# Optimization experiments

Hardware: AMD Instinct MI355X
Metric: run time of the kernel (lower is better)

Reference implementation:

```python
import jax, jax.numpy as jnp
import numpy as np

DIM = 1024
HEADS = 16
DIM_HEAD = 64
INNER = HEADS * DIM_HEAD  # 1024
SCALE = DIM_HEAD ** -0.5


def setup_inputs() -> dict:
    key = jax.random.key(0)
    k_x, k_qkv, k_ow, k_ob = jax.random.split(key, 4)
    B, N = 4, 2048
    x = jax.random.normal(k_x, (B, N, DIM), dtype=jnp.float32)
    # nn.Linear weights stored as [out, in] in torch; keep [in, out] for x @ W.
    w_qkv = jax.random.normal(k_qkv, (DIM, 3 * INNER), dtype=jnp.float32) * (DIM ** -0.5)
    w_out = jax.random.normal(k_ow, (INNER, DIM), dtype=jnp.float32) * (INNER ** -0.5)
    b_out = jax.random.normal(k_ob, (DIM,), dtype=jnp.float32) * 0.01
    return {"x": x, "w_qkv": w_qkv, "w_out": w_out, "b_out": b_out}


def reference(x, w_qkv, w_out, b_out):
    B, N, _ = x.shape
    qkv = x @ w_qkv  # [B, N, 3*inner]
    q, k, v = jnp.split(qkv, 3, axis=-1)
    # [B, N, inner] -> [B, H, N, dh]
    def to_heads(t):
        return t.reshape(B, N, HEADS, DIM_HEAD).transpose(0, 2, 1, 3)
    q, k, v = to_heads(q), to_heads(k), to_heads(v)
    attn = jnp.einsum("bhqd,bhkd->bhqk", q, k) * SCALE  # [B, H, N, N]
    attn = jax.nn.softmax(attn, axis=-1)
    out = jnp.einsum("bhqk,bhkd->bhqd", attn, v)  # [B, H, N, dh]
    out = out.transpose(0, 2, 1, 3).reshape(B, N, INNER)
    return out @ w_out + b_out
```

## Files before the change

### kernel.cpp

```cpp
#include <hip/hip_runtime.h>
#include <hip/hip_bf16.h>
#include <stdint.h>

typedef __attribute__((ext_vector_type(4))) float f32x4;
typedef __attribute__((ext_vector_type(16))) float f32x16;
typedef __attribute__((ext_vector_type(8))) short s16x8;
typedef __attribute__((ext_vector_type(4))) short s16x4;
typedef __attribute__((ext_vector_type(4))) unsigned int u32x4;

#define DEV static __device__ __forceinline__

constexpr int B_ = 4, H_ = 16, N_ = 2048;
constexpr float CL_ = 0.18033688011112042f;

DEV short f2bf(float x) {
  __hip_bfloat16 h = __float2bfloat16(x);
  return *reinterpret_cast<short*>(&h);
}

DEV uint32_t cvtpk(float lo, float hi) {
  uint32_t r;
  asm("v_cvt_pk_bf16_f32 %0, %1, %2" : "=v"(r) : "v"(lo), "v"(hi));
  return r;
}

DEV void gload16(const void* g, void* l) {
  __builtin_amdgcn_global_load_lds((const __attribute__((address_space(1))) void*)g,
                                   (__attribute__((address_space(3))) void*)l, 16, 0, 0);
}

__global__ void k_prep(const float* __restrict__ x, short* __restrict__ xb,
                       const float* __restrict__ wqkv, short* __restrict__ wqkvT,
                       const float* __restrict__ wout, short* __restrict__ woutT) {
  __shared__ short t[64][72];
  int bid = blockIdx.x, tid = threadIdx.x;
  if (bid < 4096) {
    int i = (bid * 256 + tid) * 8;
    const float4* p = reinterpret_cast<const float4*>(x + i);
    float4 a = p[0], b = p[1];
    s16x8 o;
    o[0] = f2bf(a.x); o[1] = f2bf(a.y); o[2] = f2bf(a.z); o[3] = f2bf(a.w);
    o[4] = f2bf(b.x); o[5] = f2bf(b.y); o[6] = f2bf(b.z); o[7] = f2bf(b.w);
    *reinterpret_cast<s16x8*>(xb + i) = o;
    return;
  }
  const float* W;
  short* WT;
  int R = 1024, C, r0, c0;
  if (bid < 4864) {
    int id = bid - 4096;
    W = wqkv; WT = wqkvT; C = 3072;
    c0 = (id % 48) * 64; r0 = (id / 48) * 64;
  } else {
    int id = bid - 4864;
    W = wout; WT = woutT; C = 1024;
    c0 = (id % 16) * 64; r0 = (id / 16) * 64;
  }
  int r = tid >> 2, cp = (tid & 3) * 16;
  const float4* s4 = reinterpret_cast<const float4*>(W + (size_t)(r0 + r) * C + c0 + cp);
  float4 f0 = s4[0], f1 = s4[1], f2 = s4[2], f3 = s4[3];
  short* tr = &t[r][cp];
  tr[0] = f2bf(f0.x); tr[1] = f2bf(f0.y); tr[2]  = f2bf(f0.z); tr[3]  = f2bf(f0.w);
  tr[4] = f2bf(f1.x); tr[5] = f2bf(f1.y); tr[6]  = f2bf(f1.z); tr[7]  = f2bf(f1.w);
  tr[8] = f2bf(f2.x); tr[9] = f2bf(f2.y); tr[10] = f2bf(f2.z); tr[11] = f2bf(f2.w);
  tr[12] = f2bf(f3.x); tr[13] = f2bf(f3.y); tr[14] = f2bf(f3.z); tr[15] = f2bf(f3.w);
  __syncthreads();
  int cc = tid >> 2, rp = (tid & 3) * 16;
  short buf[16];
#pragma unroll
  for (int i = 0; i < 16; ++i) buf[i] = t[rp + i][cc];
  short* dst = WT + (size_t)(c0 + cc) * R + r0 + rp;
  *reinterpret_cast<s16x8*>(dst) = *reinterpret_cast<s16x8*>(buf);
  *reinterpret_cast<s16x8*>(dst + 8) = *reinterpret_cast<s16x8*>(buf + 8);
}

__global__ __launch_bounds__(512, 2)
void k_gemm0(const short* __restrict__ A, const short* __restrict__ BT,
             short* __restrict__ oq, short* __restrict__ ok, short* __restrict__ ovT) {
  __shared__ __align__(16) char smem[98304];
  constexpr int NT = 32;
  const int tid = threadIdx.x;
  const int m0 = blockIdx.x * 128, n0 = blockIdx.y * 256;
  const int lane = tid & 63, w = tid >> 6, g = (lane >> 4) & 3, c = lane & 15;
  const int wm = w & 1, wn = w >> 1;
  f32x4 acc[4][4] = {};
  const int ra = tid >> 2, ca = (tid & 3) * 8;
  const int rb1 = ra + 128;
  const short* gA = A + (size_t)(m0 + ra) * 1024 + ca;
  const short* gB0 = BT + (size_t)(n0 + ra) * 1024 + ca;
  const short* gB1 = BT + (size_t)(n0 + rb1) * 1024 + ca;
#define STAGE0(T)                                                   \
  {                                                                 \
    char* nb = smem + ((T) & 3) * 24576;                            \
    gload16(gA + (T) * 32, nb + tid * 16);                          \
    gload16(gB0 + (T) * 32, nb + 8192 + tid * 16);                  \
    gload16(gB1 + (T) * 32, nb + 8192 + (tid + 512) * 16);          \
  }
  STAGE0(0);
  STAGE0(1);
  for (int t = 0; t < NT; ++t) {
    if (t + 1 < NT) {
      asm volatile("s_waitcnt vmcnt(3)" ::: "memory");
    } else {
      asm volatile("s_waitcnt vmcnt(0)" ::: "memory");
    }
    __builtin_amdgcn_s_barrier();
    __builtin_amdgcn_sched_barrier(0);
    if (t + 2 < NT) STAGE0(t + 2);
    const char* sb = smem + (t & 3) * 24576;
    s16x8 af[4], bf[4];
#pragma unroll
    for (int i = 0; i < 4; ++i)
      af[i] = *reinterpret_cast<const s16x8*>(sb + (wm * 64 + i * 16 + c) * 64 + g * 16);
#pragma unroll
    for (int j = 0; j < 4; ++j)
      bf[j] = *reinterpret_cast<const s16x8*>(sb + 8192 + (wn * 64 + j * 16 + c) * 64 + g * 16);
    __builtin_amdgcn_s_setprio(1);
#pragma unroll
    for (int i = 0; i < 4; ++i)
#pragma unroll
      for (int j = 0; j < 4; ++j)
        acc[i][j] = __builtin_amdgcn_mfma_f32_16x16x32_bf16(af[i], bf[j], acc[i][j], 0, 0, 0);
    __builtin_amdgcn_s_setprio(0);
  }
#undef STAGE0
#pragma unroll
  for (int j = 0; j < 4; ++j) {
    int ncol = n0 + wn * 64 + j * 16 + c;
    int part = ncol >> 10;
    int c10 = ncol & 1023;
    int h = c10 >> 6, d = c10 & 63;
    if (part == 2) {
#pragma unroll
      for (int i = 0; i < 4; ++i) {
        int mrow = m0 + wm * 64 + i * 16 + g * 4;
        int b = mrow >> 11, nr = mrow & 2047;
        uint2 pk;
        pk.x = cvtpk(acc[i][j][0], acc[i][j][1]);
        pk.y = cvtpk(acc[i][j][2], acc[i][j][3]);
        *reinterpret_cast<uint2*>(ovT + ((size_t)((b * H_ + h) * 64 + d) * N_ + nr)) = pk;
      }
    } else {
      short* dst0 = (part == 0) ? oq : ok;
      float qs = (part == 0) ? CL_ : 1.0f;
#pragma unroll
      for (int i = 0; i < 4; ++i) {
#pragma unroll
        for (int r = 0; r < 4; ++r) {
          int mrow = m0 + wm * 64 + i * 16 + g * 4 + r;
          int b = mrow >> 11, nr = mrow & 2047;
          dst0[((size_t)((b * H_ + h) * N_ + nr) << 6) + d] = f2bf(acc[i][j][r] * qs);
        }
      }
    }
  }
}

__global__ __launch_bounds__(256, 2)
void k_gemm1(const short* __restrict__ A, const short* __restrict__ BT,
             int M, int N, int K, const float* __restrict__ bias, float* __restrict__ out) {
  __shared__ short As[128 * 32];
  __shared__ short Bs[128 * 32];
  const int tid = threadIdx.x;
  const int m0 = blockIdx.x * 128, n0 = blockIdx.y * 128;
  const int lane = tid & 63, w = tid >> 6, g = lane >> 4, c = lane & 15;
  const int wr = w >> 1, wc = w & 1;
  f32x4 acc[4][4] = {};
  const int trow = tid >> 2, tk = (tid & 3) * 8;
  const short* ga = A + (size_t)(m0 + trow) * K + tk;
  const short* gb = BT + (size_t)(n0 + trow) * K + tk;
  short* la = As + tid * 8;
  short* lb = Bs + tid * 8;
  for (int k0 = 0; k0 < K; k0 += 32) {
    gload16(ga + k0, la);
    gload16(ga + (size_t)64 * K + k0, la + 2048);
    gload16(gb + k0, lb);
    gload16(gb + (size_t)64 * K + k0, lb + 2048);
    __syncthreads();
    s16x8 af[4], bf[4];
#pragma unroll
    for (int i = 0; i < 4; ++i)
      af[i] = *reinterpret_cast<const s16x8*>(As + (wr * 64 + i * 16 + c) * 32 + g * 8);
#pragma unroll
    for (int j = 0; j < 4; ++j)
      bf[j] = *reinterpret_cast<const s16x8*>(Bs + (wc * 64 + j * 16 + c) * 32 + g * 8);
#pragma unroll
    for (int i = 0; i < 4; ++i)
#pragma unroll
      for (int j = 0; j < 4; ++j)
        acc[i][j] = __builtin_amdgcn_mfma_f32_16x16x32_bf16(af[i], bf[j], acc[i][j], 0, 0, 0);
    __syncthreads();
  }
#pragma unroll
  for (int bj = 0; bj < 4; ++bj) {
    int ncol = n0 + wc * 64 + bj * 16 + c;
    float bb = bias[ncol];
#pragma unroll
    for (int ai = 0; ai < 4; ++ai) {
#pragma unroll
      for (int r = 0; r < 4; ++r) {
        int mrow = m0 + wr * 64 + ai * 16 + g * 4 + r;
        out[(size_t)mrow * N + ncol] = acc[ai][bj][r] + bb;
      }
    }
  }
}

__global__ __launch_bounds__(256, 4)
void k_attn(const short* __restrict__ q, const short* __restrict__ kk,
            const short* __restrict__ vT, short* __restrict__ ao) {
  __shared__ __align__(16) char smem[32768];
  constexpr int NT = N_ / 64;
  int bh = blockIdx.x, qb = blockIdx.y;
  int b = bh >> 4, head = bh & 15;
  int tid = threadIdx.x, w = tid >> 6, lane = tid & 63;
  int half = lane >> 5, qc = lane & 31;
  const size_t ho = (size_t)bh * (N_ * 64);
  const short* Q = q + ho;
  const char* Kc = reinterpret_cast<const char*>(kk + ho);
  const char* Vc = reinterpret_cast<const char*>(vT + ho);
  int q0w = qb * 128 + w * 32;
  s16x8 qf[4];
#pragma unroll
  for (int ks = 0; ks < 4; ++ks)
    qf[ks] = *reinterpret_cast<const s16x8*>(Q + (size_t)(q0w + qc) * 64 + ks * 16 + half * 8);
  f32x16 ot[2] = {};
  float lp0 = 0.f, lp1 = 0.f, lp2 = 0.f, lp3 = 0.f;
  const int rsw0 = ((qc ^ (qc >> 3)) & 7) << 4;
  const int rsw1 = rsw0 ^ 0x40;
  const int s_i0 = tid, s_i1 = tid + 256;
  const int s_r0 = s_i0 >> 3, s_r1 = s_i1 >> 3;
  const int s_c0 = (((s_i0 & 7) ^ ((s_r0 ^ (s_r0 >> 3)) & 7)) << 4);
  const int s_c1 = (((s_i1 & 7) ^ ((s_r1 ^ (s_r1 >> 3)) & 7)) << 4);
#define STAGE(T)                                                                       \
  {                                                                                    \
    char* nb = smem + ((T) & 1) * 16384;                                               \
    gload16(Kc + (size_t)((T) * 64 + s_r0) * 128 + s_c0, nb + s_i0 * 16);              \
    gload16(Kc + (size_t)((T) * 64 + s_r1) * 128 + s_c1, nb + s_i1 * 16);              \
    gload16(Vc + (size_t)s_r0 * 4096 + (T) * 128 + s_c0, nb + 8192 + s_i0 * 16);       \
    gload16(Vc + (size_t)s_r1 * 4096 + (T) * 128 + s_c1, nb + 8192 + s_i1 * 16);       \
  }
  STAGE(0);
  __syncthreads();
  for (int tt = 0; tt < NT; ++tt) {
    if (tt + 1 < NT) STAGE(tt + 1);
    const char* kb_ = smem + (tt & 1) * 16384;
    const char* vb_ = kb_ + 8192;
    f32x16 st[2];
#pragma unroll
    for (int j = 0; j < 2; ++j) {
      const int rs = j ? rsw1 : rsw0;
      s16x8 kfj[4];
#pragma unroll
      for (int ks = 0; ks < 4; ++ks)
        kfj[ks] = *reinterpret_cast<const s16x8*>(kb_ + (j * 32 + qc) * 128 + ((ks * 32 + half * 16) ^ rs));
      f32x16 acc = {};
      __builtin_amdgcn_s_setprio(1);
#pragma unroll
      for (int ks = 0; ks < 4; ++ks)
        acc = __builtin_amdgcn_mfma_f32_32x32x16_bf16(kfj[ks], qf[ks], acc, 0, 0, 0);
      __builtin_amdgcn_s_setprio(0);
      st[j] = acc;
    }
#pragma unroll
    for (int j = 0; j < 2; ++j)
#pragma unroll
      for (int r = 0; r < 16; ++r) {
        float p = __builtin_amdgcn_exp2f(st[j][r]);
        st[j][r] = p;
        if ((r & 3) == 0) lp0 += p;
        else if ((r & 3) == 1) lp1 += p;
        else if ((r & 3) == 2) lp2 += p;
        else lp3 += p;
      }
    u32x4 pwv[4];
#pragma unroll
    for (int j = 0; j < 2; ++j)
#pragma unroll
      for (int bb = 0; bb < 2; ++bb)
#pragma unroll
        for (int p = 0; p < 2; ++p) {
          uint32_t Aw = cvtpk(st[j][8 * bb + 2 * p], st[j][8 * bb + 2 * p + 1]);
          uint32_t Bw = cvtpk(st[j][8 * bb + 4 + 2 * p], st[j][8 * bb + 4 + 2 * p + 1]);
          asm volatile("v_permlane32_swap_b32 %0, %1" : "+v"(Aw), "+v"(Bw));
          pwv[j * 2 + bb][p] = Aw;
          pwv[j * 2 + bb][p + 2] = Bw;
        }
#pragma unroll
    for (int db = 0; db < 2; ++db) {
      const int rs = db ? rsw1 : rsw0;
      s16x8 vf[4];
#pragma unroll
      for (int kb4 = 0; kb4 < 4; ++kb4)
        vf[kb4] = *reinterpret_cast<const s16x8*>(vb_ + (db * 32 + qc) * 128 + ((kb4 * 32 + half * 16) ^ rs));
      f32x16 acc = ot[db];
      __builtin_amdgcn_s_setprio(1);
#pragma unroll
      for (int kb4 = 0; kb4 < 4; ++kb4)
        acc = __builtin_amdgcn_mfma_f32_32x32x16_bf16(
            vf[kb4], __builtin_bit_cast(s16x8, pwv[kb4]), acc, 0, 0, 0);
      __builtin_amdgcn_s_setprio(0);
      ot[db] = acc;
    }
    __syncthreads();
  }
#undef STAGE
  float lp = (lp0 + lp1) + (lp2 + lp3);
  float linv = 1.f / (lp + __shfl_xor(lp, 32, 64));
  short* Oq = reinterpret_cast<short*>(smem) + w * 2304;
#pragma unroll
  for (int db = 0; db < 2; ++db)
#pragma unroll
    for (int m = 0; m < 4; ++m) {
      uint2 pk;
      pk.x = cvtpk(ot[db][4 * m] * linv, ot[db][4 * m + 1] * linv);
      pk.y = cvtpk(ot[db][4 * m + 2] * linv, ot[db][4 * m + 3] * linv);
      *reinterpret_cast<uint2*>(Oq + qc * 72 + db * 32 + m * 8 + half * 4) = pk;
    }
  int q2 = lane >> 1, dcol = (lane & 1) * 32;
  size_t ro = (size_t)(b * N_ + q0w + q2) * 1024 + head * 64 + dcol;
#pragma unroll
  for (int ch = 0; ch < 4; ++ch) {
    s16x8 vv = *reinterpret_cast<const s16x8*>(Oq + q2 * 72 + dcol + ch * 8);
    *reinterpret_cast<s16x8*>(ao + ro + ch * 8) = vv;
  }
}

extern "C" void kernel_launch(void* const* d_in, const int* in_sizes, int n_in,
                              void* d_out, int out_size, void* d_ws, size_t ws_size,
                              hipStream_t stream) {
  const float* x = (const float*)d_in[0];
  const float* w_qkv = (const float*)d_in[1];
  const float* w_out = (const float*)d_in[2];
  const float* b_out = (const float*)d_in[3];
  float* out = (float*)d_out;
  char* ws = (char*)d_ws;
  short* xb    = (short*)(ws);
  short* wqkvT = (short*)(ws + 16777216);
  short* woutT = (short*)(ws + 23068672);
  short* qB    = (short*)(ws + 25165824);
  short* kB    = (short*)(ws + 41943040);
  short* vTT   = (short*)(ws + 75497472);
  short* ao    = xb;

  k_prep<<<5120, 256, 0, stream>>>(x, xb, w_qkv, wqkvT, w_out, woutT);
  k_gemm0<<<dim3(64, 12), 512, 0, stream>>>(xb, wqkvT, qB, kB, vTT);
  k_attn<<<dim3(64, 16), 256, 0, stream>>>(qB, kB, vTT, ao);
  k_gemm1<<<dim3(64, 8), 256, 0, stream>>>(ao, woutT, 8192, 1024, 1024, b_out, out);
}
```

Baseline: 191.1 us.

## Double-buffer both GEMMs with 128x128 tiles and async prefetch

k_gemm0 moves from a 512-thread 128x256 tile with a 4-deep ring buffer to a 256-thread 128x128 tile with a 2-stage double buffer, doubling the grid to 64x24 blocks. k_gemm1 gets the same double-buffered prefetch scheme, replacing its load-sync-compute-sync loop so the next K-slice's global loads overlap the MFMA work. The aim is to hide global load latency in the output projection and make both GEMMs share one pipeline structure. The smaller gemm0 tile lowers data reuse per block and shortens the prefetch distance, which may expose more memory latency there.

```diff
diff --git a/kernel.cpp b/kernel.cpp
--- a/kernel.cpp
+++ b/kernel.cpp
@@ -74,93 +74,11 @@
   *reinterpret_cast<s16x8*>(dst + 8) = *reinterpret_cast<s16x8*>(buf + 8);
 }
 
-__global__ __launch_bounds__(512, 2)
+__global__ __launch_bounds__(256, 2)
 void k_gemm0(const short* __restrict__ A, const short* __restrict__ BT,
              short* __restrict__ oq, short* __restrict__ ok, short* __restrict__ ovT) {
-  __shared__ __align__(16) char smem[98304];
-  constexpr int NT = 32;
-  const int tid = threadIdx.x;
-  const int m0 = blockIdx.x * 128, n0 = blockIdx.y * 256;
-  const int lane = tid & 63, w = tid >> 6, g = (lane >> 4) & 3, c = lane & 15;
-  const int wm = w & 1, wn = w >> 1;
-  f32x4 acc[4][4] = {};
-  const int ra = tid >> 2, ca = (tid & 3) * 8;
-  const int rb1 = ra + 128;
-  const short* gA = A + (size_t)(m0 + ra) * 1024 + ca;
-  const short* gB0 = BT + (size_t)(n0 + ra) * 1024 + ca;
-  const short* gB1 = BT + (size_t)(n0 + rb1) * 1024 + ca;
-#define STAGE0(T)                                                   \
-  {                                                                 \
-    char* nb = smem + ((T) & 3) * 24576;                            \
-    gload16(gA + (T) * 32, nb + tid * 16);                          \
-    gload16(gB0 + (T) * 32, nb + 8192 + tid * 16);                  \
-    gload16(gB1 + (T) * 32, nb + 8192 + (tid + 512) * 16);          \
-  }
-  STAGE0(0);
-  STAGE0(1);
-  for (int t = 0; t < NT; ++t) {
-    if (t + 1 < NT) {
-      asm volatile("s_waitcnt vmcnt(3)" ::: "memory");
-    } else {
-      asm volatile("s_waitcnt vmcnt(0)" ::: "memory");
-    }
-    __builtin_amdgcn_s_barrier();
-    __builtin_amdgcn_sched_barrier(0);
-    if (t + 2 < NT) STAGE0(t + 2);
-    const char* sb = smem + (t & 3) * 24576;
-    s16x8 af[4], bf[4];
-#pragma unroll
-    for (int i = 0; i < 4; ++i)
-      af[i] = *reinterpret_cast<const s16x8*>(sb + (wm * 64 + i * 16 + c) * 64 + g * 16);
-#pragma unroll
-    for (int j = 0; j < 4; ++j)
-      bf[j] = *reinterpret_cast<const s16x8*>(sb + 8192 + (wn * 64 + j * 16 + c) * 64 + g * 16);
-    __builtin_amdgcn_s_setprio(1);
-#pragma unroll
-    for (int i = 0; i < 4; ++i)
-#pragma unroll
-      for (int j = 0; j < 4; ++j)
-        acc[i][j] = __builtin_amdgcn_mfma_f32_16x16x32_bf16(af[i], bf[j], acc[i][j], 0, 0, 0);
-    __builtin_amdgcn_s_setprio(0);
-  }
-#undef STAGE0
-#pragma unroll
-  for (int j = 0; j < 4; ++j) {
-    int ncol = n0 + wn * 64 + j * 16 + c;
-    int part = ncol >> 10;
-    int c10 = ncol & 1023;
-    int h = c10 >> 6, d = c10 & 63;
-    if (part == 2) {
-#pragma unroll
-      for (int i = 0; i < 4; ++i) {
-        int mrow = m0 + wm * 64 + i * 16 + g * 4;
-        int b = mrow >> 11, nr = mrow & 2047;
-        uint2 pk;
-        pk.x = cvtpk(acc[i][j][0], acc[i][j][1]);
-        pk.y = cvtpk(acc[i][j][2], acc[i][j][3]);
-        *reinterpret_cast<uint2*>(ovT + ((size_t)((b * H_ + h) * 64 + d) * N_ + nr)) = pk;
-      }
-    } else {
-      short* dst0 = (part == 0) ? oq : ok;
-      float qs = (part == 0) ? CL_ : 1.0f;
-#pragma unroll
-      for (int i = 0; i < 4; ++i) {
-#pragma unroll
-        for (int r = 0; r < 4; ++r) {
-          int mrow = m0 + wm * 64 + i * 16 + g * 4 + r;
-          int b = mrow >> 11, nr = mrow & 2047;
-          dst0[((size_t)((b * H_ + h) * N_ + nr) << 6) + d] = f2bf(acc[i][j][r] * qs);
-        }
-      }
-    }
-  }
-}
-
-__global__ __launch_bounds__(256, 2)
-void k_gemm1(const short* __restrict__ A, const short* __restrict__ BT,
-             int M, int N, int K, const float* __restrict__ bias, float* __restrict__ out) {
-  __shared__ short As[128 * 32];
-  __shared__ short Bs[128 * 32];
+  __shared__ __align__(16) char smem[32768];
+  constexpr int K = 1024, NT = 32;
   const int tid = threadIdx.x;
   const int m0 = blockIdx.x * 128, n0 = blockIdx.y * 128;
   const int lane = tid & 63, w = tid >> 6, g = lane >> 4, c = lane & 15;
@@ -169,28 +87,115 @@
   const int trow = tid >> 2, tk = (tid & 3) * 8;
   const short* ga = A + (size_t)(m0 + trow) * K + tk;
   const short* gb = BT + (size_t)(n0 + trow) * K + tk;
-  short* la = As + tid * 8;
-  short* lb = Bs + tid * 8;
-  for (int k0 = 0; k0 < K; k0 += 32) {
-    gload16(ga + k0, la);
-    gload16(ga + (size_t)64 * K + k0, la + 2048);
-    gload16(gb + k0, lb);
-    gload16(gb + (size_t)64 * K + k0, lb + 2048);
-    __syncthreads();
+#define STG0(T)                                                    \
+  {                                                                \
+    char* nb = smem + ((T) & 1) * 16384;                           \
+    gload16(ga + (T) * 32, nb + tid * 16);                         \
+    gload16(ga + (size_t)64 * K + (T) * 32, nb + 4096 + tid * 16); \
+    gload16(gb + (T) * 32, nb + 8192 + tid * 16);                  \
+    gload16(gb + (size_t)64 * K + (T) * 32, nb + 12288 + tid * 16);\
+  }
+  STG0(0);
+  asm volatile("s_waitcnt vmcnt(0)" ::: "memory");
+  __builtin_amdgcn_s_barrier();
+  for (int t = 0; t < NT; ++t) {
+    if (t + 1 < NT) STG0(t + 1);
+    const char* sb = smem + (t & 1) * 16384;
     s16x8 af[4], bf[4];
 #pragma unroll
     for (int i = 0; i < 4; ++i)
-      af[i] = *reinterpret_cast<const s16x8*>(As + (wr * 64 + i * 16 + c) * 32 + g * 8);
+      af[i] = *reinterpret_cast<const s16x8*>(sb + (wr * 64 + i * 16 + c) * 64 + g * 16);
 #pragma unroll
     for (int j = 0; j < 4; ++j)
-      bf[j] = *reinterpret_cast<const s16x8*>(Bs + (wc * 64 + j * 16 + c) * 32 + g * 8);
+      bf[j] = *reinterpret_cast<const s16x8*>(sb + 8192 + (wc * 64 + j * 16 + c) * 64 + g * 16);
+    __builtin_amdgcn_s_setprio(1);
 #pragma unroll
     for (int i = 0; i < 4; ++i)
 #pragma unroll
       for (int j = 0; j < 4; ++j)
         acc[i][j] = __builtin_amdgcn_mfma_f32_16x16x32_bf16(af[i], bf[j], acc[i][j], 0, 0, 0);
-    __syncthreads();
-  }
+    __builtin_amdgcn_s_setprio(0);
+    asm volatile("s_waitcnt vmcnt(0)" ::: "memory");
+    __builtin_amdgcn_s_barrier();
+  }
+#undef STG0
+#pragma unroll
+  for (int bj = 0; bj < 4; ++bj) {
+    int ncol = n0 + wc * 64 + bj * 16 + c;
+    int part = ncol >> 10;
+    int c10 = ncol & 1023;
+    int h = c10 >> 6, d = c10 & 63;
+    if (part == 2) {
+#pragma unroll
+      for (int ai = 0; ai < 4; ++ai) {
+        int mrow = m0 + wr * 64 + ai * 16 + g * 4;
+        int b = mrow >> 11, nr = mrow & 2047;
+        uint2 pk;
+        pk.x = cvtpk(acc[ai][bj][0], acc[ai][bj][1]);
+        pk.y = cvtpk(acc[ai][bj][2], acc[ai][bj][3]);
+        *reinterpret_cast<uint2*>(ovT + ((size_t)((b * H_ + h) * 64 + d) * N_ + nr)) = pk;
+      }
+    } else {
+      short* dst0 = (part == 0) ? oq : ok;
+      float qs = (part == 0) ? CL_ : 1.0f;
+#pragma unroll
+      for (int ai = 0; ai < 4; ++ai) {
+#pragma unroll
+        for (int r = 0; r < 4; ++r) {
+          int mrow = m0 + wr * 64 + ai * 16 + g * 4 + r;
+          int b = mrow >> 11, nr = mrow & 2047;
+          dst0[((size_t)((b * H_ + h) * N_ + nr) << 6) + d] = f2bf(acc[ai][bj][r] * qs);
+        }
+      }
+    }
+  }
+}
+
+__global__ __launch_bounds__(256, 2)
+void k_gemm1(const short* __restrict__ A, const short* __restrict__ BT,
+             int M, int N, int K, const float* __restrict__ bias, float* __restrict__ out) {
+  __shared__ __align__(16) char smem[32768];
+  const int NT = K / 32;
+  const int tid = threadIdx.x;
+  const int m0 = blockIdx.x * 128, n0 = blockIdx.y * 128;
+  const int lane = tid & 63, w = tid >> 6, g = lane >> 4, c = lane & 15;
+  const int wr = w >> 1, wc = w & 1;
+  f32x4 acc[4][4] = {};
+  const int trow = tid >> 2, tk = (tid & 3) * 8;
+  const short* ga = A + (size_t)(m0 + trow) * K + tk;
+  const short* gb = BT + (size_t)(n0 + trow) * K + tk;
+#define STG1(T)                                                    \
+  {                                                                \
+    char* nb = smem + ((T) & 1) * 16384;                           \
+    gload16(ga + (T) * 32, nb + tid * 16);                         \
+    gload16(ga + (size_t)64 * K + (T) * 32, nb + 4096 + tid * 16); \
+    gload16(gb + (T) * 32, nb + 8192 + tid * 16);                  \
+    gload16(gb + (size_t)64 * K + (T) * 32, nb + 12288 + tid * 16);\
+  }
+  STG1(0);
+  asm volatile("s_waitcnt vmcnt(0)" ::: "memory");
+  __builtin_amdgcn_s_barrier();
+  for (int t = 0; t < NT; ++t) {
+    if (t + 1 < NT) STG1(t + 1);
+    const char* sb = smem + (t & 1) * 16384;
+    s16x8 af[4], bf[4];
+#pragma unroll
+    for (int i = 0; i < 4; ++i)
+      af[i] = *reinterpret_cast<const s16x8*>(sb + (wr * 64 + i * 16 + c) * 64 + g * 16);
+#pragma unroll
+    for (int j = 0; j < 4; ++j)
+      bf[j] = *reinterpret_cast<const s16x8*>(sb + 8192 + (wc * 64 + j * 16 + c) * 64 + g * 16);
+    __builtin_amdgcn_s_setprio(1);
+#pragma unroll
+    for (int i = 0; i < 4; ++i)
+#pragma unroll
+      for (int j = 0; j < 4; ++j)
+        acc[i][j] = __builtin_amdgcn_mfma_f32_16x16x32_bf16(af[i], bf[j], acc[i][j], 0, 0, 0);
+    __builtin_amdgcn_s_setprio(0);
+    asm volatile("s_waitcnt vmcnt(0)" ::: "memory");
+    __builtin_amdgcn_s_barrier();
+  }
+#undef STG1
 #pragma unroll
   for (int bj = 0; bj < 4; ++bj) {
     int ncol = n0 + wc * 64 + bj * 16 + c;
@@ -344,7 +349,7 @@
   short* ao    = xb;
 
   k_prep<<<5120, 256, 0, stream>>>(x, xb, w_qkv, wqkvT, w_out, woutT);
-  k_gemm0<<<dim3(64, 12), 512, 0, stream>>>(xb, wqkvT, qB, kB, vTT);
+  k_gemm0<<<dim3(64, 24), 256, 0, stream>>>(xb, wqkvT, qB, kB, vTT);
   k_attn<<<dim3(64, 16), 256, 0, stream>>>(qB, kB, vTT, ao);
   k_gemm1<<<dim3(64, 8), 256, 0, stream>>>(ao, woutT, 8192, 1024, 1024, b_out, out);
 }
```

Result: no change. 188.1 us, median of 2 (-1.6%).
